# Kernel tuning notes

Hardware: AMD Instinct MI355X
Metric: run time of the kernel (lower is better)

## Reference

```python
import jax, jax.numpy as jnp
import numpy as np

DIM = 1024
H = 16
HD = DIM // H
EPS = 1e-5


def setup_inputs() -> dict:
    key = jax.random.key(0)
    ks = jax.random.split(key, 12)
    B, S = 4, 2048
    s = 0.02
    return {
        "q": jax.random.normal(ks[0], (B, S, DIM), jnp.float32),
        "k": jax.random.normal(ks[1], (B, S, DIM), jnp.float32),
        "v": jax.random.normal(ks[2], (B, S, DIM), jnp.float32),
        "Wq": jax.random.normal(ks[3], (DIM, DIM), jnp.float32) * s,
        "bq": jnp.zeros((DIM,), jnp.float32),
        "Wk": jax.random.normal(ks[4], (DIM, DIM), jnp.float32) * s,
        "bk": jnp.zeros((DIM,), jnp.float32),
        "Wv": jax.random.normal(ks[5], (DIM, DIM), jnp.float32) * s,
        "bv": jnp.zeros((DIM,), jnp.float32),
        "Wo": jax.random.normal(ks[6], (DIM, DIM), jnp.float32) * s,
        "bo": jnp.zeros((DIM,), jnp.float32),
        "gamma": jnp.ones((DIM,), jnp.float32),
        "beta": jnp.zeros((DIM,), jnp.float32),
    }


def reference(q, k, v, Wq, bq, Wk, bk, Wv, bv, Wo, bo, gamma, beta):
    B, S, _ = q.shape
    scale = HD ** -0.5
    # projections -> [B, H, S, HD]
    def proj(x, W, b):
        return (x @ W.T + b).reshape(B, -1, H, HD).transpose(0, 2, 1, 3)
    qh = proj(q, Wq, bq)
    kh = proj(k, Wk, bk)
    vh = proj(v, Wv, bv)
    scores = jnp.einsum("bhsd,bhtd->bhst", qh, kh) * scale  # [B,H,S,S]
    attn = jax.nn.softmax(scores, axis=-1)  # dropout is identity in eval
    out = jnp.einsum("bhst,bhtd->bhsd", attn, vh)
    out = out.transpose(0, 2, 1, 3).reshape(B, S, DIM)
    out = out @ Wo.T + bo
    # LayerNorm
    mu = out.mean(-1, keepdims=True)
    var = out.var(-1, keepdims=True)
    return (out - mu) * jax.lax.rsqrt(var + EPS) * gamma + beta
```

## Files before the change

### kernel.cpp

```cpp
#include <hip/hip_runtime.h>

typedef unsigned short u16;
typedef __attribute__((ext_vector_type(8))) short bf16x8;
typedef __attribute__((ext_vector_type(4))) float f32x4;
typedef __attribute__((ext_vector_type(16))) float f32x16;
typedef __attribute__((ext_vector_type(4))) unsigned short u16x4;
typedef __attribute__((ext_vector_type(4))) unsigned int u32x4;
typedef __attribute__((ext_vector_type(2))) unsigned int u32x2;

#define DIM 1024
#define NH 16
#define HD 64
#define BATCH 4
#define SEQ 2048
#define MROWS (BATCH * SEQ)

__device__ __forceinline__ u16 f2bf(float f) {
  unsigned u = __builtin_bit_cast(unsigned, f);
  return (u16)((u + 0x7fffu + ((u >> 16) & 1u)) >> 16);
}

__device__ __forceinline__ void gload16(const u16* g, u16* l) {
  __builtin_amdgcn_global_load_lds(
      (const __attribute__((address_space(1))) void*)g,
      (__attribute__((address_space(3))) void*)l, 16, 0, 0);
}

__device__ __forceinline__ unsigned cvtpk(float lo, float hi) {
  unsigned r;
  asm("v_cvt_pk_bf16_f32 %0, %1, %2" : "=v"(r) : "v"(lo), "v"(hi));
  return r;
}

__device__ __forceinline__ void plswap(unsigned& a, unsigned& b) {
  asm("v_permlane32_swap_b32 %0, %1" : "+v"(a), "+v"(b));
}

__global__ __launch_bounds__(256) void cvtw_kernel(const float* __restrict__ Wq,
                                                   const float* __restrict__ Wk,
                                                   const float* __restrict__ Wv,
                                                   const float* __restrict__ Wo,
                                                   u16* __restrict__ dst,
                                                   float scale) {
  int i = blockIdx.x * blockDim.x + threadIdx.x;
  int seg = i >> 18;
  int off = i & ((1 << 18) - 1);
  const float* src = (seg == 0) ? Wq : (seg == 1) ? Wk : (seg == 2) ? Wv : Wo;
  float mul = (seg == 0) ? scale : 1.f;
  f32x4 v = ((const f32x4*)src)[off];
  u16x4 o;
  o[0] = f2bf(v[0] * mul);
  o[1] = f2bf(v[1] * mul);
  o[2] = f2bf(v[2] * mul);
  o[3] = f2bf(v[3] * mul);
  ((u16x4*)dst)[i] = o;
}

enum { EPI_QK = 0, EPI_VT = 1, EPI_F32 = 2 };

#define BM 128
#define BN 128
#define BK 64

template <int EPI, bool AF32, bool BF32, int DEC>
__global__ __launch_bounds__(256) void gemm_nt(const void* __restrict__ Ap,
                                               const void* __restrict__ Bp,
                                               void* __restrict__ C,
                                               const float* __restrict__ bias,
                                               float bscale, int Kdim) {
  __shared__ __attribute__((aligned(16))) u16 Alds[2][BM * BK];
  __shared__ __attribute__((aligned(16))) u16 Blds[2][BN * BK];

  const int tid = threadIdx.x;
  const int w = tid >> 6, l = tid & 63;
  const int wr = w >> 1, wc = w & 1;
  const int p = blockIdx.x;
  const int row0 = (DEC == 0 ? (p & 63) : (p >> 6)) * BM;
  const int col0 = (DEC == 0 ? (p >> 6) : (p & 63)) * BN;
  const int lr = l >> 3;
  const int sp = l & 7;
  const int sl = sp ^ lr;

  f32x4 acc[4][4];
#pragma unroll
  for (int i = 0; i < 4; i++)
#pragma unroll
    for (int j = 0; j < 4; j++) {
      f32x4 z = {0.f, 0.f, 0.f, 0.f};
      acc[i][j] = z;
    }

  f32x4 stA[4][2], stB[4][2];

  auto stage_issue = [&](int k0, int buf) {
#pragma unroll
    for (int q = 0; q < 4; q++) {
      int chunk = w * 4 + q;
      int r = chunk * 8 + lr;
      if constexpr (AF32) {
        const float* s =
            (const float*)Ap + (size_t)(row0 + r) * Kdim + k0 + sp * 8;
        stA[q][0] = *(const f32x4*)s;
        stA[q][1] = *(const f32x4*)(s + 4);
      } else {
        gload16((const u16*)Ap + (size_t)(row0 + r) * Kdim + k0 + sl * 8,
                &Alds[buf][chunk * 512]);
      }
      if constexpr (BF32) {
        const float* s =
            (const float*)Bp + (size_t)(col0 + r) * Kdim + k0 + sp * 8;
        stB[q][0] = *(const f32x4*)s;
        stB[q][1] = *(const f32x4*)(s + 4);
      } else {
        gload16((const u16*)Bp + (size_t)(col0 + r) * Kdim + k0 + sl * 8,
                &Blds[buf][chunk * 512]);
      }
    }
  };

  auto stage_write = [&](int buf) {
    if constexpr (AF32) {
#pragma unroll
      for (int q = 0; q < 4; q++) {
        int r = (w * 4 + q) * 8 + lr;
        u32x4 pk;
        pk[0] = cvtpk(stA[q][0][0], stA[q][0][1]);
        pk[1] = cvtpk(stA[q][0][2], stA[q][0][3]);
        pk[2] = cvtpk(stA[q][1][0], stA[q][1][1]);
        pk[3] = cvtpk(stA[q][1][2], stA[q][1][3]);
        *(u32x4*)&Alds[buf][r * 64 + sl * 8] = pk;
      }
    }
    if constexpr (BF32) {
#pragma unroll
      for (int q = 0; q < 4; q++) {
        int r = (w * 4 + q) * 8 + lr;
        u32x4 pk;
        pk[0] = cvtpk(stB[q][0][0], stB[q][0][1]);
        pk[1] = cvtpk(stB[q][0][2], stB[q][0][3]);
        pk[2] = cvtpk(stB[q][1][0], stB[q][1][1]);
        pk[3] = cvtpk(stB[q][1][2], stB[q][1][3]);
        *(u32x4*)&Blds[buf][r * 64 + sl * 8] = pk;
      }
    }
  };

  stage_issue(0, 0);
  asm volatile("s_waitcnt vmcnt(0)" ::: "memory");
  stage_write(0);
  __syncthreads();

  const int NT = Kdim / BK;
  int cur = 0;
  for (int kt = 0; kt < NT; kt++) {
    if (kt < NT - 1) stage_issue((kt + 1) * BK, cur ^ 1);

    const u16* Ab = Alds[cur];
    const u16* Bb = Blds[cur];
#pragma unroll
    for (int t = 0; t < 2; t++) {
      int slot = (t * 4 + (l >> 4)) ^ (l & 7);
      bf16x8 af[4], bf[4];
#pragma unroll
      for (int i = 0; i < 4; i++) {
        int arow = wr * 64 + i * 16 + (l & 15);
        af[i] = *(const bf16x8*)&Ab[arow * 64 + slot * 8];
        int brow = wc * 64 + i * 16 + (l & 15);
        bf[i] = *(const bf16x8*)&Bb[brow * 64 + slot * 8];
      }
      __builtin_amdgcn_s_setprio(1);
#pragma unroll
      for (int i = 0; i < 4; i++)
#pragma unroll
        for (int j = 0; j < 4; j++)
          acc[i][j] = __builtin_amdgcn_mfma_f32_16x16x32_bf16(af[i], bf[j],
                                                              acc[i][j], 0, 0, 0);
      __builtin_amdgcn_s_setprio(0);
    }

    if (kt < NT - 1) {
      asm volatile("s_waitcnt vmcnt(0)" ::: "memory");
      stage_write(cur ^ 1);
      __syncthreads();
      cur ^= 1;
    }
  }

#pragma unroll
  for (int i = 0; i < 4; i++) {
#pragma unroll
    for (int j = 0; j < 4; j++) {
#pragma unroll
      for (int q = 0; q < 4; q++) {
        int m = row0 + wr * 64 + i * 16 + (l >> 4) * 4 + q;
        int n = col0 + wc * 64 + j * 16 + (l & 15);
        float v = acc[i][j][q];
        if (EPI == EPI_QK) {
          v += bias[n] * bscale;
          int b_ = m >> 11, s_ = m & (SEQ - 1), h_ = n >> 6, hd_ = n & 63;
          ((u16*)C)[(((size_t)(b_ * NH + h_) * SEQ + s_) << 6) + hd_] = f2bf(v);
        } else if (EPI == EPI_VT) {
          v += bias[m];
          int b_ = n >> 11, s_ = n & (SEQ - 1);
          ((u16*)C)[((size_t)(b_ * NH + (m >> 6)) * HD + (m & 63)) * SEQ + s_] =
              f2bf(v);
        } else {
          v += bias[n];
          ((float*)C)[(size_t)m * DIM + n] = v;
        }
      }
    }
  }
}

__global__ __launch_bounds__(256, 2) void attn_kernel(const u16* __restrict__ Qh,
                                                      const u16* __restrict__ Kh,
                                                      const u16* __restrict__ Vt,
                                                      u16* __restrict__ AO) {
  __shared__ __attribute__((aligned(16))) u16 Klds[3][64 * 64];
  __shared__ __attribute__((aligned(16))) u16 Vlds[3][64 * 64];

  const int tid = threadIdx.x;
  const int w = tid >> 6, l = tid & 63;
  const int l31 = l & 31, hi = l >> 5;
  const int p = blockIdx.x;
  const int bh = (p & 7) + 8 * (p >> 6);
  const int qt = (p >> 3) & 7;
  const int b_ = bh >> 4, h_ = bh & 15;
  const int lr = l >> 3, sp = l & 7;

  const int qrowA = qt * 256 + w * 64 + l31;
  const int qrowB = qrowA + 32;
  const u16* qpA = Qh + ((size_t)bh * SEQ + qrowA) * HD + hi * 8;
  const u16* qpB = Qh + ((size_t)bh * SEQ + qrowB) * HD + hi * 8;
  bf16x8 qfA[4], qfB[4];
#pragma unroll
  for (int ks = 0; ks < 4; ks++) {
    qfA[ks] = *(const bf16x8*)(qpA + ks * 16);
    qfB[ks] = *(const bf16x8*)(qpB + ks * 16);
  }

  f32x16 oA0, oA1, oB0, oB1;
#pragma unroll
  for (int r = 0; r < 16; r++) {
    oA0[r] = 0.f;
    oA1[r] = 0.f;
    oB0[r] = 0.f;
    oB1[r] = 0.f;
  }
  float lrunA = 0.f, lrunB = 0.f;

  const int chunk = w * 2;
  const int r0 = chunk * 8 + lr, r1 = r0 + 8;
  const int sl0 = sp ^ (lr & 7);
  const size_t kbase = (size_t)bh * SEQ * HD;
  const size_t vbase = (size_t)bh * HD * SEQ;

#define ISSUE(kt, buf)                                                        \
  do {                                                                        \
    gload16(Kh + kbase + ((kt) * 64 + r0) * HD + sl0 * 8,                     \
            &Klds[buf][chunk * 512]);                                         \
    gload16(Vt + vbase + (size_t)r0 * SEQ + (kt) * 64 + sl0 * 8,              \
            &Vlds[buf][chunk * 512]);                                         \
    gload16(Kh + kbase + ((kt) * 64 + r1) * HD + sl0 * 8,                     \
            &Klds[buf][chunk * 512 + 512]);                                   \
    gload16(Vt + vbase + (size_t)r1 * SEQ + (kt) * 64 + sl0 * 8,              \
            &Vlds[buf][chunk * 512 + 512]);                                   \
  } while (0)

  ISSUE(0, 0);

  int cur = 0;
  for (int kt = 0; kt < SEQ / 64; kt++) {
    const int nxt = (cur == 2) ? 0 : cur + 1;
    if (kt < SEQ / 64 - 1) {
      ISSUE(kt + 1, nxt);
      asm volatile("s_waitcnt vmcnt(4)" ::: "memory");
    } else {
      asm volatile("s_waitcnt vmcnt(0)" ::: "memory");
    }
    __builtin_amdgcn_s_barrier();
    __builtin_amdgcn_sched_barrier(0);

    const u16* Kc = Klds[cur];
    const u16* Vc = Vlds[cur];

    f32x16 sA0, sA1, sB0, sB1;
#pragma unroll
    for (int r = 0; r < 16; r++) {
      sA0[r] = 0.f;
      sA1[r] = 0.f;
      sB0[r] = 0.f;
      sB1[r] = 0.f;
    }
    __builtin_amdgcn_s_setprio(1);
#pragma unroll
    for (int ks = 0; ks < 4; ks++) {
      int slot = ((ks * 2 + hi) ^ (l & 7)) * 8;
      bf16x8 kf0 = *(const bf16x8*)&Kc[l31 * 64 + slot];
      bf16x8 kf1 = *(const bf16x8*)&Kc[(32 + l31) * 64 + slot];
      sA0 = __builtin_amdgcn_mfma_f32_32x32x16_bf16(kf0, qfA[ks], sA0, 0, 0, 0);
      sA1 = __builtin_amdgcn_mfma_f32_32x32x16_bf16(kf1, qfA[ks], sA1, 0, 0, 0);
      sB0 = __builtin_amdgcn_mfma_f32_32x32x16_bf16(kf0, qfB[ks], sB0, 0, 0, 0);
      sB1 = __builtin_amdgcn_mfma_f32_32x32x16_bf16(kf1, qfB[ks], sB1, 0, 0, 0);
    }
    __builtin_amdgcn_s_setprio(0);

#pragma unroll
    for (int r = 0; r < 16; r++) {
      sA0[r] = __builtin_amdgcn_exp2f(sA0[r]);
      sA1[r] = __builtin_amdgcn_exp2f(sA1[r]);
      sB0[r] = __builtin_amdgcn_exp2f(sB0[r]);
      sB1[r] = __builtin_amdgcn_exp2f(sB1[r]);
    }
    float ta[16], tb[16];
#pragma unroll
    for (int r = 0; r < 8; r++) {
      ta[r] = sA0[2 * r] + sA0[2 * r + 1];
      ta[8 + r] = sA1[2 * r] + sA1[2 * r + 1];
      tb[r] = sB0[2 * r] + sB0[2 * r + 1];
      tb[8 + r] = sB1[2 * r] + sB1[2 * r + 1];
    }
#pragma unroll
    for (int s2 = 8; s2 > 0; s2 >>= 1)
#pragma unroll
      for (int r = 0; r < 8; r++)
        if (r < s2) {
          ta[r] += ta[r + s2];
          tb[r] += tb[r + s2];
        }
    float psA = ta[0];
    float psB = tb[0];
    psA += __shfl_xor(psA, 32);
    psB += __shfl_xor(psB, 32);
    lrunA += psA;
    lrunB += psB;

    unsigned cwA[2][4][2], cwB[2][4][2];
#pragma unroll
    for (int g = 0; g < 4; g++) {
      cwA[0][g][0] = cvtpk(sA0[4 * g], sA0[4 * g + 1]);
      cwA[0][g][1] = cvtpk(sA0[4 * g + 2], sA0[4 * g + 3]);
      cwA[1][g][0] = cvtpk(sA1[4 * g], sA1[4 * g + 1]);
      cwA[1][g][1] = cvtpk(sA1[4 * g + 2], sA1[4 * g + 3]);
      cwB[0][g][0] = cvtpk(sB0[4 * g], sB0[4 * g + 1]);
      cwB[0][g][1] = cvtpk(sB0[4 * g + 2], sB0[4 * g + 3]);
      cwB[1][g][0] = cvtpk(sB1[4 * g], sB1[4 * g + 1]);
      cwB[1][g][1] = cvtpk(sB1[4 * g + 2], sB1[4 * g + 3]);
    }
    bf16x8 paA[4], paB[4];
#pragma unroll
    for (int ks = 0; ks < 4; ks++) {
      int t = ks >> 1, c = ks & 1;
      {
        unsigned a0 = cwA[t][2 * c][0], b0 = cwA[t][2 * c + 1][0];
        unsigned a1 = cwA[t][2 * c][1], b1 = cwA[t][2 * c + 1][1];
        plswap(a0, b0);
        plswap(a1, b1);
        u32x4 pw;
        pw[0] = a0;
        pw[1] = a1;
        pw[2] = b0;
        pw[3] = b1;
        paA[ks] = __builtin_bit_cast(bf16x8, pw);
      }
      {
        unsigned a0 = cwB[t][2 * c][0], b0 = cwB[t][2 * c + 1][0];
        unsigned a1 = cwB[t][2 * c][1], b1 = cwB[t][2 * c + 1][1];
        plswap(a0, b0);
        plswap(a1, b1);
        u32x4 pw;
        pw[0] = a0;
        pw[1] = a1;
        pw[2] = b0;
        pw[3] = b1;
        paB[ks] = __builtin_bit_cast(bf16x8, pw);
      }
    }

    __builtin_amdgcn_s_setprio(1);
#pragma unroll
    for (int ks = 0; ks < 4; ks++) {
      int slot = ((ks * 2 + hi) ^ (l & 7)) * 8;
      bf16x8 vf0 = *(const bf16x8*)&Vc[l31 * 64 + slot];
      bf16x8 vf1 = *(const bf16x8*)&Vc[(32 + l31) * 64 + slot];
      oA0 = __builtin_amdgcn_mfma_f32_32x32x16_bf16(vf0, paA[ks], oA0, 0, 0, 0);
      oA1 = __builtin_amdgcn_mfma_f32_32x32x16_bf16(vf1, paA[ks], oA1, 0, 0, 0);
      oB0 = __builtin_amdgcn_mfma_f32_32x32x16_bf16(vf0, paB[ks], oB0, 0, 0, 0);
      oB1 = __builtin_amdgcn_mfma_f32_32x32x16_bf16(vf1, paB[ks], oB1, 0, 0, 0);
    }
    __builtin_amdgcn_s_setprio(0);

    cur = nxt;
  }

  float rinvA = 1.f / lrunA;
  float rinvB = 1.f / lrunB;
  u16* orowA = AO + ((size_t)b_ * SEQ + qrowA) * DIM + h_ * HD;
  u16* orowB = AO + ((size_t)b_ * SEQ + qrowB) * DIM + h_ * HD;
#pragma unroll
  for (int g = 0; g < 4; g++) {
    u32x2 s0, s1;
    s0[0] = cvtpk(oA0[4 * g] * rinvA, oA0[4 * g + 1] * rinvA);
    s0[1] = cvtpk(oA0[4 * g + 2] * rinvA, oA0[4 * g + 3] * rinvA);
    s1[0] = cvtpk(oA1[4 * g] * rinvA, oA1[4 * g + 1] * rinvA);
    s1[1] = cvtpk(oA1[4 * g + 2] * rinvA, oA1[4 * g + 3] * rinvA);
    *(u32x2*)(orowA + 8 * g + 4 * hi) = s0;
    *(u32x2*)(orowA + 32 + 8 * g + 4 * hi) = s1;
    s0[0] = cvtpk(oB0[4 * g] * rinvB, oB0[4 * g + 1] * rinvB);
    s0[1] = cvtpk(oB0[4 * g + 2] * rinvB, oB0[4 * g + 3] * rinvB);
    s1[0] = cvtpk(oB1[4 * g] * rinvB, oB1[4 * g + 1] * rinvB);
    s1[1] = cvtpk(oB1[4 * g + 2] * rinvB, oB1[4 * g + 3] * rinvB);
    *(u32x2*)(orowB + 8 * g + 4 * hi) = s0;
    *(u32x2*)(orowB + 32 + 8 * g + 4 * hi) = s1;
  }
}

__global__ __launch_bounds__(256) void ln_kernel(const float* __restrict__ X,
                                                 const float* __restrict__ gamma,
                                                 const float* __restrict__ beta,
                                                 float* __restrict__ out) {
  __shared__ float red[8];
  const int row = blockIdx.x;
  const int tid = threadIdx.x;
  const float* xr = X + (size_t)row * DIM;
  f32x4 v = ((const f32x4*)xr)[tid];
  float s = v[0] + v[1] + v[2] + v[3];
  float ss = v[0] * v[0] + v[1] * v[1] + v[2] * v[2] + v[3] * v[3];
#pragma unroll
  for (int mm = 1; mm <= 32; mm <<= 1) {
    s += __shfl_xor(s, mm);
    ss += __shfl_xor(ss, mm);
  }
  const int w = tid >> 6, l = tid & 63;
  if (l == 0) {
    red[w * 2] = s;
    red[w * 2 + 1] = ss;
  }
  __syncthreads();
  s = red[0] + red[2] + red[4] + red[6];
  ss = red[1] + red[3] + red[5] + red[7];
  float mu = s * (1.f / DIM);
  float var = ss * (1.f / DIM) - mu * mu;
  float rstd = rsqrtf(var + 1e-5f);
  f32x4 g = ((const f32x4*)gamma)[tid];
  f32x4 bt = ((const f32x4*)beta)[tid];
  f32x4 o;
#pragma unroll
  for (int j = 0; j < 4; j++) o[j] = (v[j] - mu) * rstd * g[j] + bt[j];
  ((f32x4*)(out + (size_t)row * DIM))[tid] = o;
}

extern "C" void kernel_launch(void* const* d_in, const int* in_sizes, int n_in,
                              void* d_out, int out_size, void* d_ws,
                              size_t ws_size, hipStream_t stream) {
  (void)in_sizes; (void)n_in; (void)out_size; (void)ws_size;
  const float* q = (const float*)d_in[0];
  const float* k = (const float*)d_in[1];
  const float* v = (const float*)d_in[2];
  const float* Wq = (const float*)d_in[3];
  const float* bq = (const float*)d_in[4];
  const float* Wk = (const float*)d_in[5];
  const float* bk = (const float*)d_in[6];
  const float* Wv = (const float*)d_in[7];
  const float* bv = (const float*)d_in[8];
  const float* Wo = (const float*)d_in[9];
  const float* bo = (const float*)d_in[10];
  const float* gamma = (const float*)d_in[11];
  const float* beta = (const float*)d_in[12];

  char* ws = (char*)d_ws;
  const size_t MiB = 1 << 20;
  u16* Wb = (u16*)(ws + 0 * MiB);
  u16* Wq_b = Wb;
  u16* Wk_b = (u16*)(ws + 2 * MiB);
  u16* Wv_b = (u16*)(ws + 4 * MiB);
  u16* Wo_b = (u16*)(ws + 6 * MiB);
  u16* Qh = (u16*)(ws + 8 * MiB);
  u16* Kh = (u16*)(ws + 24 * MiB);
  u16* Vt = (u16*)(ws + 40 * MiB);
  u16* AO = (u16*)(ws + 56 * MiB);

  const float scale = 0.125f * 1.44269504088896f;

  cvtw_kernel<<<4096, 256, 0, stream>>>(Wq, Wk, Wv, Wo, Wb, scale);

  dim3 blk(256);
  gemm_nt<EPI_QK, true, false, 0><<<512, blk, 0, stream>>>(q, Wq_b, Qh, bq,
                                                           scale, DIM);
  gemm_nt<EPI_QK, true, false, 0><<<512, blk, 0, stream>>>(k, Wk_b, Kh, bk,
                                                           1.f, DIM);
  gemm_nt<EPI_VT, false, true, 1><<<512, blk, 0, stream>>>(Wv_b, v, Vt, bv,
                                                           1.f, DIM);

  attn_kernel<<<512, blk, 0, stream>>>(Qh, Kh, Vt, AO);

  gemm_nt<EPI_F32, false, false, 0><<<512, blk, 0, stream>>>(
      AO, Wo_b, (float*)d_out, bo, 1.f, DIM);

  ln_kernel<<<MROWS, 256, 0, stream>>>((const float*)d_out, gamma, beta,
                                       (float*)d_out);
}
```

Measured before the change: 203.6 us.

## Split attention over two key halves and merge partials in output GEMM

Attention runs as 1024 blocks, each handling half of the key sequence. Each block writes an unnormalized bf16 partial output and its row sums. The output-projection GEMM loads both partials and the two row sums and forms the normalized sum while staging A into LDS. The goal is more parallelism and occupancy (launch bounds 4, double rather than triple buffering) in exchange for extra partial-output traffic. The path depends on workspace size, and it relies on no-max softmax, which risks bf16 precision loss in the unnormalized partials.

After: 569.5 us. 2.8x slower.

```diff
diff --git a/kernel.cpp b/kernel.cpp
--- a/kernel.cpp
+++ b/kernel.cpp
@@ -18,6 +18,13 @@
 __device__ __forceinline__ u16 f2bf(float f) {
   unsigned u = __builtin_bit_cast(unsigned, f);
   return (u16)((u + 0x7fffu + ((u >> 16) & 1u)) >> 16);
+}
+
+__device__ __forceinline__ float bflo(unsigned w) {
+  return __builtin_bit_cast(float, w << 16);
+}
+__device__ __forceinline__ float bfhi(unsigned w) {
+  return __builtin_bit_cast(float, w & 0xffff0000u);
 }
 
 __device__ __forceinline__ void gload16(const u16* g, u16* l) {
@@ -62,12 +69,13 @@
 #define BN 128
 #define BK 64
 
-template <int EPI, bool AF32, bool BF32, int DEC>
-__global__ __launch_bounds__(256) void gemm_nt(const void* __restrict__ Ap,
-                                               const void* __restrict__ Bp,
-                                               void* __restrict__ C,
-                                               const float* __restrict__ bias,
-                                               float bscale, int Kdim) {
+template <int EPI, bool AF32, bool BF32, int DEC, bool ACMB = false>
+__global__ __launch_bounds__(256) void gemm_nt(
+    const void* __restrict__ Ap, const void* __restrict__ Bp,
+    void* __restrict__ C, const float* __restrict__ bias, float bscale,
+    int Kdim, const u16* __restrict__ A2 = nullptr,
+    const float* __restrict__ L1 = nullptr,
+    const float* __restrict__ L2 = nullptr) {
   __shared__ __attribute__((aligned(16))) u16 Alds[2][BM * BK];
   __shared__ __attribute__((aligned(16))) u16 Blds[2][BN * BK];
 
@@ -91,13 +99,21 @@
     }
 
   f32x4 stA[4][2], stB[4][2];
+  u32x4 stU1[4], stU2[4];
+  float stl[4];
 
   auto stage_issue = [&](int k0, int buf) {
 #pragma unroll
     for (int q = 0; q < 4; q++) {
       int chunk = w * 4 + q;
       int r = chunk * 8 + lr;
-      if constexpr (AF32) {
+      if constexpr (ACMB) {
+        size_t off = (size_t)(row0 + r) * Kdim + k0 + sp * 8;
+        stU1[q] = *(const u32x4*)((const u16*)Ap + off);
+        stU2[q] = *(const u32x4*)(A2 + off);
+        stl[q] = 1.f / (L1[(row0 + r) * NH + (k0 >> 6)] +
+                        L2[(row0 + r) * NH + (k0 >> 6)]);
+      } else if constexpr (AF32) {
         const float* s =
             (const float*)Ap + (size_t)(row0 + r) * Kdim + k0 + sp * 8;
         stA[q][0] = *(const f32x4*)s;
@@ -119,7 +135,21 @@
   };
 
   auto stage_write = [&](int buf) {
-    if constexpr (AF32) {
+    if constexpr (ACMB) {
+#pragma unroll
+      for (int q = 0; q < 4; q++) {
+        int r = (w * 4 + q) * 8 + lr;
+        float n = stl[q];
+        u32x4 pk;
+#pragma unroll
+        for (int jj = 0; jj < 4; jj++) {
+          float lo = (bflo(stU1[q][jj]) + bflo(stU2[q][jj])) * n;
+          float hi = (bfhi(stU1[q][jj]) + bfhi(stU2[q][jj])) * n;
+          pk[jj] = cvtpk(lo, hi);
+        }
+        *(u32x4*)&Alds[buf][r * 64 + sl * 8] = pk;
+      }
+    } else if constexpr (AF32) {
 #pragma unroll
       for (int q = 0; q < 4; q++) {
         int r = (w * 4 + q) * 8 + lr;
@@ -213,21 +243,26 @@
   }
 }
 
-__global__ __launch_bounds__(256, 2) void attn_kernel(const u16* __restrict__ Qh,
-                                                      const u16* __restrict__ Kh,
-                                                      const u16* __restrict__ Vt,
-                                                      u16* __restrict__ AO) {
-  __shared__ __attribute__((aligned(16))) u16 Klds[3][64 * 64];
-  __shared__ __attribute__((aligned(16))) u16 Vlds[3][64 * 64];
+__global__ __launch_bounds__(256, 4) void attn_split_kernel(
+    const u16* __restrict__ Qh, const u16* __restrict__ Kh,
+    const u16* __restrict__ Vt, u16* __restrict__ AO1,
+    u16* __restrict__ AO2, float* __restrict__ L1, float* __restrict__ L2) {
+  __shared__ __attribute__((aligned(16))) u16 Klds[2][64 * 64];
+  __shared__ __attribute__((aligned(16))) u16 Vlds[2][64 * 64];
 
   const int tid = threadIdx.x;
   const int w = tid >> 6, l = tid & 63;
   const int l31 = l & 31, hi = l >> 5;
   const int p = blockIdx.x;
-  const int bh = (p & 7) + 8 * (p >> 6);
+  const int bh = (p & 7) + 8 * (p >> 7);
   const int qt = (p >> 3) & 7;
+  const int half = (p >> 6) & 1;
   const int b_ = bh >> 4, h_ = bh & 15;
   const int lr = l >> 3, sp = l & 7;
+
+  u16* U = half ? AO2 : AO1;
+  float* Lh = half ? L2 : L1;
+  const int kt0 = half * 16;
 
   const int qrowA = qt * 256 + w * 64 + l31;
   const int qrowB = qrowA + 32;
@@ -267,6 +302,200 @@
     gload16(Vt + vbase + (size_t)r1 * SEQ + (kt) * 64 + sl0 * 8,              \
             &Vlds[buf][chunk * 512 + 512]);                                   \
   } while (0)
+
+  ISSUE(kt0, 0);
+
+  for (int i = 0; i < 16; i++) {
+    const int cur = i & 1;
+    if (i < 15) {
+      ISSUE(kt0 + i + 1, cur ^ 1);
+      asm volatile("s_waitcnt vmcnt(4)" ::: "memory");
+    } else {
+      asm volatile("s_waitcnt vmcnt(0)" ::: "memory");
+    }
+    __builtin_amdgcn_s_barrier();
+    __builtin_amdgcn_sched_barrier(0);
+
+    const u16* Kc = Klds[cur];
+    const u16* Vc = Vlds[cur];
+
+    f32x16 sA0, sA1, sB0, sB1;
+#pragma unroll
+    for (int r = 0; r < 16; r++) {
+      sA0[r] = 0.f;
+      sA1[r] = 0.f;
+      sB0[r] = 0.f;
+      sB1[r] = 0.f;
+    }
+    __builtin_amdgcn_s_setprio(1);
+#pragma unroll
+    for (int ks = 0; ks < 4; ks++) {
+      int slot = ((ks * 2 + hi) ^ (l & 7)) * 8;
+      bf16x8 kf0 = *(const bf16x8*)&Kc[l31 * 64 + slot];
+      bf16x8 kf1 = *(const bf16x8*)&Kc[(32 + l31) * 64 + slot];
+      sA0 = __builtin_amdgcn_mfma_f32_32x32x16_bf16(kf0, qfA[ks], sA0, 0, 0, 0);
+      sA1 = __builtin_amdgcn_mfma_f32_32x32x16_bf16(kf1, qfA[ks], sA1, 0, 0, 0);
+      sB0 = __builtin_amdgcn_mfma_f32_32x32x16_bf16(kf0, qfB[ks], sB0, 0, 0, 0);
+      sB1 = __builtin_amdgcn_mfma_f32_32x32x16_bf16(kf1, qfB[ks], sB1, 0, 0, 0);
+    }
+    __builtin_amdgcn_s_setprio(0);
+
+#pragma unroll
+    for (int r = 0; r < 16; r++) {
+      sA0[r] = __builtin_amdgcn_exp2f(sA0[r]);
+      sA1[r] = __builtin_amdgcn_exp2f(sA1[r]);
+      sB0[r] = __builtin_amdgcn_exp2f(sB0[r]);
+      sB1[r] = __builtin_amdgcn_exp2f(sB1[r]);
+    }
+    float ta[16], tb[16];
+#pragma unroll
+    for (int r = 0; r < 8; r++) {
+      ta[r] = sA0[2 * r] + sA0[2 * r + 1];
+      ta[8 + r] = sA1[2 * r] + sA1[2 * r + 1];
+      tb[r] = sB0[2 * r] + sB0[2 * r + 1];
+      tb[8 + r] = sB1[2 * r] + sB1[2 * r + 1];
+    }
+#pragma unroll
+    for (int s2 = 8; s2 > 0; s2 >>= 1)
+#pragma unroll
+      for (int r = 0; r < 8; r++)
+        if (r < s2) {
+          ta[r] += ta[r + s2];
+          tb[r] += tb[r + s2];
+        }
+    float psA = ta[0];
+    float psB = tb[0];
+    psA += __shfl_xor(psA, 32);
+    psB += __shfl_xor(psB, 32);
+    lrunA += psA;
+    lrunB += psB;
+
+    unsigned cwA[2][4][2], cwB[2][4][2];
+#pragma unroll
+    for (int g = 0; g < 4; g++) {
+      cwA[0][g][0] = cvtpk(sA0[4 * g], sA0[4 * g + 1]);
+      cwA[0][g][1] = cvtpk(sA0[4 * g + 2], sA0[4 * g + 3]);
+      cwA[1][g][0] = cvtpk(sA1[4 * g], sA1[4 * g + 1]);
+      cwA[1][g][1] = cvtpk(sA1[4 * g + 2], sA1[4 * g + 3]);
+      cwB[0][g][0] = cvtpk(sB0[4 * g], sB0[4 * g + 1]);
+      cwB[0][g][1] = cvtpk(sB0[4 * g + 2], sB0[4 * g + 3]);
+      cwB[1][g][0] = cvtpk(sB1[4 * g], sB1[4 * g + 1]);
+      cwB[1][g][1] = cvtpk(sB1[4 * g + 2], sB1[4 * g + 3]);
+    }
+    bf16x8 paA[4], paB[4];
+#pragma unroll
+    for (int ks = 0; ks < 4; ks++) {
+      int t = ks >> 1, c = ks & 1;
+      {
+        unsigned a0 = cwA[t][2 * c][0], b0 = cwA[t][2 * c + 1][0];
+        unsigned a1 = cwA[t][2 * c][1], b1 = cwA[t][2 * c + 1][1];
+        plswap(a0, b0);
+        plswap(a1, b1);
+        u32x4 pw;
+        pw[0] = a0;
+        pw[1] = a1;
+        pw[2] = b0;
+        pw[3] = b1;
+        paA[ks] = __builtin_bit_cast(bf16x8, pw);
+      }
+      {
+        unsigned a0 = cwB[t][2 * c][0], b0 = cwB[t][2 * c + 1][0];
+        unsigned a1 = cwB[t][2 * c][1], b1 = cwB[t][2 * c + 1][1];
+        plswap(a0, b0);
+        plswap(a1, b1);
+        u32x4 pw;
+        pw[0] = a0;
+        pw[1] = a1;
+        pw[2] = b0;
+        pw[3] = b1;
+        paB[ks] = __builtin_bit_cast(bf16x8, pw);
+      }
+    }
+
+    __builtin_amdgcn_s_setprio(1);
+#pragma unroll
+    for (int ks = 0; ks < 4; ks++) {
+      int slot = ((ks * 2 + hi) ^ (l & 7)) * 8;
+      bf16x8 vf0 = *(const bf16x8*)&Vc[l31 * 64 + slot];
+      bf16x8 vf1 = *(const bf16x8*)&Vc[(32 + l31) * 64 + slot];
+      oA0 = __builtin_amdgcn_mfma_f32_32x32x16_bf16(vf0, paA[ks], oA0, 0, 0, 0);
+      oA1 = __builtin_amdgcn_mfma_f32_32x32x16_bf16(vf1, paA[ks], oA1, 0, 0, 0);
+      oB0 = __builtin_amdgcn_mfma_f32_32x32x16_bf16(vf0, paB[ks], oB0, 0, 0, 0);
+      oB1 = __builtin_amdgcn_mfma_f32_32x32x16_bf16(vf1, paB[ks], oB1, 0, 0, 0);
+    }
+    __builtin_amdgcn_s_setprio(0);
+
+    asm volatile("" ::: "memory");
+    __builtin_amdgcn_s_barrier();
+    __builtin_amdgcn_sched_barrier(0);
+  }
+
+  u16* orowA = U + ((size_t)b_ * SEQ + qrowA) * DIM + h_ * HD;
+  u16* orowB = U + ((size_t)b_ * SEQ + qrowB) * DIM + h_ * HD;
+#pragma unroll
+  for (int g = 0; g < 4; g++) {
+    u32x2 s0, s1;
+    s0[0] = cvtpk(oA0[4 * g], oA0[4 * g + 1]);
+    s0[1] = cvtpk(oA0[4 * g + 2], oA0[4 * g + 3]);
+    s1[0] = cvtpk(oA1[4 * g], oA1[4 * g + 1]);
+    s1[1] = cvtpk(oA1[4 * g + 2], oA1[4 * g + 3]);
+    *(u32x2*)(orowA + 8 * g + 4 * hi) = s0;
+    *(u32x2*)(orowA + 32 + 8 * g + 4 * hi) = s1;
+    s0[0] = cvtpk(oB0[4 * g], oB0[4 * g + 1]);
+    s0[1] = cvtpk(oB0[4 * g + 2], oB0[4 * g + 3]);
+    s1[0] = cvtpk(oB1[4 * g], oB1[4 * g + 1]);
+    s1[1] = cvtpk(oB1[4 * g + 2], oB1[4 * g + 3]);
+    *(u32x2*)(orowB + 8 * g + 4 * hi) = s0;
+    *(u32x2*)(orowB + 32 + 8 * g + 4 * hi) = s1;
+  }
+  if (!hi) {
+    Lh[((size_t)b_ * SEQ + qrowA) * NH + h_] = lrunA;
+    Lh[((size_t)b_ * SEQ + qrowB) * NH + h_] = lrunB;
+  }
+}
+
+__global__ __launch_bounds__(256, 2) void attn_kernel(const u16* __restrict__ Qh,
+                                                      const u16* __restrict__ Kh,
+                                                      const u16* __restrict__ Vt,
+                                                      u16* __restrict__ AO) {
+  __shared__ __attribute__((aligned(16))) u16 Klds[3][64 * 64];
+  __shared__ __attribute__((aligned(16))) u16 Vlds[3][64 * 64];
+
+  const int tid = threadIdx.x;
+  const int w = tid >> 6, l = tid & 63;
+  const int l31 = l & 31, hi = l >> 5;
+  const int p = blockIdx.x;
+  const int bh = (p & 7) + 8 * (p >> 6);
+  const int qt = (p >> 3) & 7;
+  const int b_ = bh >> 4, h_ = bh & 15;
+  const int lr = l >> 3, sp = l & 7;
+
+  const int qrowA = qt * 256 + w * 64 + l31;
+  const int qrowB = qrowA + 32;
+  const u16* qpA = Qh + ((size_t)bh * SEQ + qrowA) * HD + hi * 8;
+  const u16* qpB = Qh + ((size_t)bh * SEQ + qrowB) * HD + hi * 8;
+  bf16x8 qfA[4], qfB[4];
+#pragma unroll
+  for (int ks = 0; ks < 4; ks++) {
+    qfA[ks] = *(const bf16x8*)(qpA + ks * 16);
+    qfB[ks] = *(const bf16x8*)(qpB + ks * 16);
+  }
+
+  f32x16 oA0, oA1, oB0, oB1;
+#pragma unroll
+  for (int r = 0; r < 16; r++) {
+    oA0[r] = 0.f;
+    oA1[r] = 0.f;
+    oB0[r] = 0.f;
+    oB1[r] = 0.f;
+  }
+  float lrunA = 0.f, lrunB = 0.f;
+
+  const int chunk = w * 2;
+  const int r0 = chunk * 8 + lr, r1 = r0 + 8;
+  const int sl0 = sp ^ (lr & 7);
+  const size_t kbase = (size_t)bh * SEQ * HD;
+  const size_t vbase = (size_t)bh * HD * SEQ;
 
   ISSUE(0, 0);
 
@@ -454,7 +683,7 @@
 extern "C" void kernel_launch(void* const* d_in, const int* in_sizes, int n_in,
                               void* d_out, int out_size, void* d_ws,
                               size_t ws_size, hipStream_t stream) {
-  (void)in_sizes; (void)n_in; (void)out_size; (void)ws_size;
+  (void)in_sizes; (void)n_in; (void)out_size;
   const float* q = (const float*)d_in[0];
   const float* k = (const float*)d_in[1];
   const float* v = (const float*)d_in[2];
@@ -479,7 +708,12 @@
   u16* Qh = (u16*)(ws + 8 * MiB);
   u16* Kh = (u16*)(ws + 24 * MiB);
   u16* Vt = (u16*)(ws + 40 * MiB);
-  u16* AO = (u16*)(ws + 56 * MiB);
+  u16* AO1 = (u16*)(ws + 56 * MiB);
+  u16* AO2 = (u16*)(ws + 72 * MiB);
+  float* L1 = (float*)(ws + 88 * MiB);
+  float* L2 = (float*)(ws + 88 * MiB + 512 * 1024);
+
+  const bool split = ws_size >= 90 * MiB;
 
   const float scale = 0.125f * 1.44269504088896f;
 
@@ -493,10 +727,15 @@
   gemm_nt<EPI_VT, false, true, 1><<<512, blk, 0, stream>>>(Wv_b, v, Vt, bv,
                                                            1.f, DIM);
 
-  attn_kernel<<<512, blk, 0, stream>>>(Qh, Kh, Vt, AO);
-
-  gemm_nt<EPI_F32, false, false, 0><<<512, blk, 0, stream>>>(
-      AO, Wo_b, (float*)d_out, bo, 1.f, DIM);
+  if (split) {
+    attn_split_kernel<<<1024, blk, 0, stream>>>(Qh, Kh, Vt, AO1, AO2, L1, L2);
+    gemm_nt<EPI_F32, false, false, 0, true><<<512, blk, 0, stream>>>(
+        AO1, Wo_b, (float*)d_out, bo, 1.f, DIM, AO2, L1, L2);
+  } else {
+    attn_kernel<<<512, blk, 0, stream>>>(Qh, Kh, Vt, AO1);
+    gemm_nt<EPI_F32, false, false, 0><<<512, blk, 0, stream>>>(
+        AO1, Wo_b, (float*)d_out, bo, 1.f, DIM);
+  }
 
   ln_kernel<<<MROWS, 256, 0, stream>>>((const float*)d_out, gamma, beta,
                                        (float*)d_out);
```

## Split attention over two KV halves and merge partials in output projection

Applied to the files above, without the earlier changes.

The attention kernel now splits each (batch, head, query-tile) job into two blocks, each covering half of the key/value sequence. Each block writes an unnormalized partial output and its softmax denominator. The output-projection GEMM gains a combine mode: it loads both partials, adds them, and scales by the inverse summed denominators before staging into LDS. The intent is to double the number of attention blocks for better CU fill. The cost is extra partial-output traffic, extra combine work in the GEMM, and a K/V pipeline cut from triple to double buffering with a per-iteration barrier. The merge applies no per-half max correction, so it is only correct if both halves share the same softmax offset.

Measured after the change: 266.4 us. +30.9%, slower.

```diff
diff --git a/kernel.cpp b/kernel.cpp
--- a/kernel.cpp
+++ b/kernel.cpp
@@ -18,6 +18,13 @@
 __device__ __forceinline__ u16 f2bf(float f) {
   unsigned u = __builtin_bit_cast(unsigned, f);
   return (u16)((u + 0x7fffu + ((u >> 16) & 1u)) >> 16);
+}
+
+__device__ __forceinline__ float bflo(unsigned w) {
+  return __builtin_bit_cast(float, w << 16);
+}
+__device__ __forceinline__ float bfhi(unsigned w) {
+  return __builtin_bit_cast(float, w & 0xffff0000u);
 }
 
 __device__ __forceinline__ void gload16(const u16* g, u16* l) {
@@ -62,12 +69,13 @@
 #define BN 128
 #define BK 64
 
-template <int EPI, bool AF32, bool BF32, int DEC>
-__global__ __launch_bounds__(256) void gemm_nt(const void* __restrict__ Ap,
-                                               const void* __restrict__ Bp,
-                                               void* __restrict__ C,
-                                               const float* __restrict__ bias,
-                                               float bscale, int Kdim) {
+template <int EPI, bool AF32, bool BF32, int DEC, bool ACMB = false>
+__global__ __launch_bounds__(256) void gemm_nt(
+    const void* __restrict__ Ap, const void* __restrict__ Bp,
+    void* __restrict__ C, const float* __restrict__ bias, float bscale,
+    int Kdim, const u16* __restrict__ A2 = nullptr,
+    const float* __restrict__ L1 = nullptr,
+    const float* __restrict__ L2 = nullptr) {
   __shared__ __attribute__((aligned(16))) u16 Alds[2][BM * BK];
   __shared__ __attribute__((aligned(16))) u16 Blds[2][BN * BK];
 
@@ -91,13 +99,21 @@
     }
 
   f32x4 stA[4][2], stB[4][2];
+  u32x4 stU1[4], stU2[4];
+  float stl[4];
 
   auto stage_issue = [&](int k0, int buf) {
 #pragma unroll
     for (int q = 0; q < 4; q++) {
       int chunk = w * 4 + q;
       int r = chunk * 8 + lr;
-      if constexpr (AF32) {
+      if constexpr (ACMB) {
+        size_t off = (size_t)(row0 + r) * Kdim + k0 + sp * 8;
+        stU1[q] = *(const u32x4*)((const u16*)Ap + off);
+        stU2[q] = *(const u32x4*)(A2 + off);
+        stl[q] = 1.f / (L1[(row0 + r) * NH + (k0 >> 6)] +
+                        L2[(row0 + r) * NH + (k0 >> 6)]);
+      } else if constexpr (AF32) {
         const float* s =
             (const float*)Ap + (size_t)(row0 + r) * Kdim + k0 + sp * 8;
         stA[q][0] = *(const f32x4*)s;
@@ -119,7 +135,21 @@
   };
 
   auto stage_write = [&](int buf) {
-    if constexpr (AF32) {
+    if constexpr (ACMB) {
+#pragma unroll
+      for (int q = 0; q < 4; q++) {
+        int r = (w * 4 + q) * 8 + lr;
+        float n = stl[q];
+        u32x4 pk;
+#pragma unroll
+        for (int jj = 0; jj < 4; jj++) {
+          float lo = (bflo(stU1[q][jj]) + bflo(stU2[q][jj])) * n;
+          float hi = (bfhi(stU1[q][jj]) + bfhi(stU2[q][jj])) * n;
+          pk[jj] = cvtpk(lo, hi);
+        }
+        *(u32x4*)&Alds[buf][r * 64 + sl * 8] = pk;
+      }
+    } else if constexpr (AF32) {
 #pragma unroll
       for (int q = 0; q < 4; q++) {
         int r = (w * 4 + q) * 8 + lr;
@@ -213,21 +243,26 @@
   }
 }
 
-__global__ __launch_bounds__(256, 2) void attn_kernel(const u16* __restrict__ Qh,
-                                                      const u16* __restrict__ Kh,
-                                                      const u16* __restrict__ Vt,
-                                                      u16* __restrict__ AO) {
-  __shared__ __attribute__((aligned(16))) u16 Klds[3][64 * 64];
-  __shared__ __attribute__((aligned(16))) u16 Vlds[3][64 * 64];
+__global__ __launch_bounds__(256) void attn_split_kernel(
+    const u16* __restrict__ Qh, const u16* __restrict__ Kh,
+    const u16* __restrict__ Vt, u16* __restrict__ AO1,
+    u16* __restrict__ AO2, float* __restrict__ L1, float* __restrict__ L2) {
+  __shared__ __attribute__((aligned(16))) u16 Klds[2][64 * 64];
+  __shared__ __attribute__((aligned(16))) u16 Vlds[2][64 * 64];
 
   const int tid = threadIdx.x;
   const int w = tid >> 6, l = tid & 63;
   const int l31 = l & 31, hi = l >> 5;
   const int p = blockIdx.x;
-  const int bh = (p & 7) + 8 * (p >> 6);
+  const int bh = (p & 7) + 8 * (p >> 7);
   const int qt = (p >> 3) & 7;
+  const int half = (p >> 6) & 1;
   const int b_ = bh >> 4, h_ = bh & 15;
   const int lr = l >> 3, sp = l & 7;
+
+  u16* U = half ? AO2 : AO1;
+  float* Lh = half ? L2 : L1;
+  const int kt0 = half * 16;
 
   const int qrowA = qt * 256 + w * 64 + l31;
   const int qrowB = qrowA + 32;
@@ -268,13 +303,12 @@
             &Vlds[buf][chunk * 512 + 512]);                                   \
   } while (0)
 
-  ISSUE(0, 0);
-
-  int cur = 0;
-  for (int kt = 0; kt < SEQ / 64; kt++) {
-    const int nxt = (cur == 2) ? 0 : cur + 1;
-    if (kt < SEQ / 64 - 1) {
-      ISSUE(kt + 1, nxt);
+  ISSUE(kt0, 0);
+
+  for (int i = 0; i < 16; i++) {
+    const int cur = i & 1;
+    if (i < 15) {
+      ISSUE(kt0 + i + 1, cur ^ 1);
       asm volatile("s_waitcnt vmcnt(4)" ::: "memory");
     } else {
       asm volatile("s_waitcnt vmcnt(0)" ::: "memory");
@@ -391,28 +425,32 @@
     }
     __builtin_amdgcn_s_setprio(0);
 
-    cur = nxt;
-  }
-
-  float rinvA = 1.f / lrunA;
-  float rinvB = 1.f / lrunB;
-  u16* orowA = AO + ((size_t)b_ * SEQ + qrowA) * DIM + h_ * HD;
-  u16* orowB = AO + ((size_t)b_ * SEQ + qrowB) * DIM + h_ * HD;
+    asm volatile("" ::: "memory");
+    __builtin_amdgcn_s_barrier();
+    __builtin_amdgcn_sched_barrier(0);
+  }
+
+  u16* orowA = U + ((size_t)b_ * SEQ + qrowA) * DIM + h_ * HD;
+  u16* orowB = U + ((size_t)b_ * SEQ + qrowB) * DIM + h_ * HD;
 #pragma unroll
   for (int g = 0; g < 4; g++) {
     u32x2 s0, s1;
-    s0[0] = cvtpk(oA0[4 * g] * rinvA, oA0[4 * g + 1] * rinvA);
-    s0[1] = cvtpk(oA0[4 * g + 2] * rinvA, oA0[4 * g + 3] * rinvA);
-    s1[0] = cvtpk(oA1[4 * g] * rinvA, oA1[4 * g + 1] * rinvA);
-    s1[1] = cvtpk(oA1[4 * g + 2] * rinvA, oA1[4 * g + 3] * rinvA);
+    s0[0] = cvtpk(oA0[4 * g], oA0[4 * g + 1]);
+    s0[1] = cvtpk(oA0[4 * g + 2], oA0[4 * g + 3]);
+    s1[0] = cvtpk(oA1[4 * g], oA1[4 * g + 1]);
+    s1[1] = cvtpk(oA1[4 * g + 2], oA1[4 * g + 3]);
     *(u32x2*)(orowA + 8 * g + 4 * hi) = s0;
     *(u32x2*)(orowA + 32 + 8 * g + 4 * hi) = s1;
-    s0[0] = cvtpk(oB0[4 * g] * rinvB, oB0[4 * g + 1] * rinvB);
-    s0[1] = cvtpk(oB0[4 * g + 2] * rinvB, oB0[4 * g + 3] * rinvB);
-    s1[0] = cvtpk(oB1[4 * g] * rinvB, oB1[4 * g + 1] * rinvB);
-    s1[1] = cvtpk(oB1[4 * g + 2] * rinvB, oB1[4 * g + 3] * rinvB);
+    s0[0] = cvtpk(oB0[4 * g], oB0[4 * g + 1]);
+    s0[1] = cvtpk(oB0[4 * g + 2], oB0[4 * g + 3]);
+    s1[0] = cvtpk(oB1[4 * g], oB1[4 * g + 1]);
+    s1[1] = cvtpk(oB1[4 * g + 2], oB1[4 * g + 3]);
     *(u32x2*)(orowB + 8 * g + 4 * hi) = s0;
     *(u32x2*)(orowB + 32 + 8 * g + 4 * hi) = s1;
+  }
+  if (!hi) {
+    Lh[((size_t)b_ * SEQ + qrowA) * NH + h_] = lrunA;
+    Lh[((size_t)b_ * SEQ + qrowB) * NH + h_] = lrunB;
   }
 }
 
@@ -479,7 +517,10 @@
   u16* Qh = (u16*)(ws + 8 * MiB);
   u16* Kh = (u16*)(ws + 24 * MiB);
   u16* Vt = (u16*)(ws + 40 * MiB);
-  u16* AO = (u16*)(ws + 56 * MiB);
+  u16* AO1 = (u16*)(ws + 56 * MiB);
+  u16* AO2 = (u16*)(ws + 72 * MiB);
+  float* L1 = (float*)(ws + 88 * MiB);
+  float* L2 = (float*)(ws + 88 * MiB + 512 * 1024);
 
   const float scale = 0.125f * 1.44269504088896f;
 
@@ -493,10 +534,9 @@
   gemm_nt<EPI_VT, false, true, 1><<<512, blk, 0, stream>>>(Wv_b, v, Vt, bv,
                                                            1.f, DIM);
 
-  attn_kernel<<<512, blk, 0, stream>>>(Qh, Kh, Vt, AO);
-
-  gemm_nt<EPI_F32, false, false, 0><<<512, blk, 0, stream>>>(
-      AO, Wo_b, (float*)d_out, bo, 1.f, DIM);
+  attn_split_kernel<<<1024, blk, 0, stream>>>(Qh, Kh, Vt, AO1, AO2, L1, L2);
+  gemm_nt<EPI_F32, false, false, 0, true><<<512, blk, 0, stream>>>(
+      AO1, Wo_b, (float*)d_out, bo, 1.f, DIM, AO2, L1, L2);
 
   ln_kernel<<<MROWS, 256, 0, stream>>>((const float*)d_out, gamma, beta,
                                        (float*)d_out);
```

## Merge Q/K projection launches and compute softmax row sums via MFMA

Applied to the files above, without the earlier changes.

Fuses the Q and K projection GEMMs into a single launch of 1024 blocks, where the upper half of the grid switches to the K operands. This cuts one launch and its tail effect. In the attention kernel, the per-tile scalar reduction and shuffle for the softmax denominator is replaced with extra MFMAs against a ones vector, accumulating row sums on the matrix unit. This adds two MFMAs per k-step and two accumulator registers of 16 floats each, which raises register pressure. The sum is also taken from the bf16-rounded probabilities rather than the fp32 values.

Result: no change. 205.0 us (+0.7%).

```diff
diff --git a/kernel.cpp b/kernel.cpp
--- a/kernel.cpp
+++ b/kernel.cpp
@@ -62,19 +62,28 @@
 #define BN 128
 #define BK 64
 
-template <int EPI, bool AF32, bool BF32, int DEC>
-__global__ __launch_bounds__(256) void gemm_nt(const void* __restrict__ Ap,
-                                               const void* __restrict__ Bp,
-                                               void* __restrict__ C,
-                                               const float* __restrict__ bias,
-                                               float bscale, int Kdim) {
+template <int EPI, bool AF32, bool BF32, int DEC, bool DUAL = false>
+__global__ __launch_bounds__(256) void gemm_nt(
+    const void* Ap, const void* Bp, void* C, const float* bias, float bscale,
+    int Kdim, const void* Ap2 = nullptr, const void* Bp2 = nullptr,
+    void* C2 = nullptr, const float* bias2 = nullptr, float bscale2 = 1.f) {
   __shared__ __attribute__((aligned(16))) u16 Alds[2][BM * BK];
   __shared__ __attribute__((aligned(16))) u16 Blds[2][BN * BK];
 
   const int tid = threadIdx.x;
   const int w = tid >> 6, l = tid & 63;
   const int wr = w >> 1, wc = w & 1;
-  const int p = blockIdx.x;
+  int p = blockIdx.x;
+  if constexpr (DUAL) {
+    if (p >= 512) {
+      p -= 512;
+      Ap = Ap2;
+      Bp = Bp2;
+      C = C2;
+      bias = bias2;
+      bscale = bscale2;
+    }
+  }
   const int row0 = (DEC == 0 ? (p & 63) : (p >> 6)) * BM;
   const int col0 = (DEC == 0 ? (p >> 6) : (p & 63)) * BN;
   const int lr = l >> 3;
@@ -240,15 +249,20 @@
     qfB[ks] = *(const bf16x8*)(qpB + ks * 16);
   }
 
-  f32x16 oA0, oA1, oB0, oB1;
+  u32x4 ow;
+  ow[0] = ow[1] = ow[2] = ow[3] = 0x3f803f80u;
+  const bf16x8 onesf = __builtin_bit_cast(bf16x8, ow);
+
+  f32x16 oA0, oA1, oB0, oB1, lsA, lsB;
 #pragma unroll
   for (int r = 0; r < 16; r++) {
     oA0[r] = 0.f;
     oA1[r] = 0.f;
     oB0[r] = 0.f;
     oB1[r] = 0.f;
-  }
-  float lrunA = 0.f, lrunB = 0.f;
+    lsA[r] = 0.f;
+    lsB[r] = 0.f;
+  }
 
   const int chunk = w * 2;
   const int r0 = chunk * 8 + lr, r1 = r0 + 8;
@@ -313,28 +327,6 @@
       sB0[r] = __builtin_amdgcn_exp2f(sB0[r]);
       sB1[r] = __builtin_amdgcn_exp2f(sB1[r]);
     }
-    float ta[16], tb[16];
-#pragma unroll
-    for (int r = 0; r < 8; r++) {
-      ta[r] = sA0[2 * r] + sA0[2 * r + 1];
-      ta[8 + r] = sA1[2 * r] + sA1[2 * r + 1];
-      tb[r] = sB0[2 * r] + sB0[2 * r + 1];
-      tb[8 + r] = sB1[2 * r] + sB1[2 * r + 1];
-    }
-#pragma unroll
-    for (int s2 = 8; s2 > 0; s2 >>= 1)
-#pragma unroll
-      for (int r = 0; r < 8; r++)
-        if (r < s2) {
-          ta[r] += ta[r + s2];
-          tb[r] += tb[r + s2];
-        }
-    float psA = ta[0];
-    float psB = tb[0];
-    psA += __shfl_xor(psA, 32);
-    psB += __shfl_xor(psB, 32);
-    lrunA += psA;
-    lrunB += psB;
 
     unsigned cwA[2][4][2], cwB[2][4][2];
 #pragma unroll
@@ -388,14 +380,16 @@
       oA1 = __builtin_amdgcn_mfma_f32_32x32x16_bf16(vf1, paA[ks], oA1, 0, 0, 0);
       oB0 = __builtin_amdgcn_mfma_f32_32x32x16_bf16(vf0, paB[ks], oB0, 0, 0, 0);
       oB1 = __builtin_amdgcn_mfma_f32_32x32x16_bf16(vf1, paB[ks], oB1, 0, 0, 0);
+      lsA = __builtin_amdgcn_mfma_f32_32x32x16_bf16(onesf, paA[ks], lsA, 0, 0, 0);
+      lsB = __builtin_amdgcn_mfma_f32_32x32x16_bf16(onesf, paB[ks], lsB, 0, 0, 0);
     }
     __builtin_amdgcn_s_setprio(0);
 
     cur = nxt;
   }
 
-  float rinvA = 1.f / lrunA;
-  float rinvB = 1.f / lrunB;
+  float rinvA = 1.f / lsA[0];
+  float rinvB = 1.f / lsB[0];
   u16* orowA = AO + ((size_t)b_ * SEQ + qrowA) * DIM + h_ * HD;
   u16* orowB = AO + ((size_t)b_ * SEQ + qrowB) * DIM + h_ * HD;
 #pragma unroll
@@ -486,10 +480,8 @@
   cvtw_kernel<<<4096, 256, 0, stream>>>(Wq, Wk, Wv, Wo, Wb, scale);
 
   dim3 blk(256);
-  gemm_nt<EPI_QK, true, false, 0><<<512, blk, 0, stream>>>(q, Wq_b, Qh, bq,
-                                                           scale, DIM);
-  gemm_nt<EPI_QK, true, false, 0><<<512, blk, 0, stream>>>(k, Wk_b, Kh, bk,
-                                                           1.f, DIM);
+  gemm_nt<EPI_QK, true, false, 0, true><<<1024, blk, 0, stream>>>(
+      q, Wq_b, Qh, bq, scale, DIM, k, Wk_b, Kh, bk, 1.f);
   gemm_nt<EPI_VT, false, true, 1><<<512, blk, 0, stream>>>(Wv_b, v, Vt, bv,
                                                            1.f, DIM);
 
```
